# Optimization experiments

Hardware: AMD Instinct MI355X
Metric: run time of the kernel (lower is better)

## Reference

```python
import jax, jax.numpy as jnp
import numpy as np


def setup_inputs() -> dict:
    key = jax.random.key(0)
    ks = jax.random.split(key, 5)
    B, C, H, W = 8, 64, 64, 64
    Ci = 32  # inter_channels = in_channels // 2
    s = 1.0 / np.sqrt(C)
    return {
        "x": jax.random.normal(ks[0], (B, C, H, W), jnp.float32),
        "Wg": jax.random.normal(ks[1], (Ci, C), jnp.float32) * s,
        "bg": jnp.zeros((Ci,), jnp.float32),
        "Wt": jax.random.normal(ks[2], (Ci, C), jnp.float32) * s,
        "bt": jnp.zeros((Ci,), jnp.float32),
        "Wp": jax.random.normal(ks[3], (Ci, C), jnp.float32) * s,
        "bp": jnp.zeros((Ci,), jnp.float32),
        "Ww": jax.random.normal(ks[4], (C, Ci), jnp.float32) * (1.0 / np.sqrt(Ci)),
        "bw": jnp.zeros((C,), jnp.float32),
    }


def _proj(x, Wc, bc):
    # 1x1 conv: (B,C,H,W) -> (B,O,H,W), then flatten spatial -> (B,O,N)
    b, c, h, w = x.shape
    y = jnp.einsum("oc,bchw->bohw", Wc, x) + bc[None, :, None, None]
    return y.reshape(b, Wc.shape[0], h * w)


def reference(x, Wg, bg, Wt, bt, Wp, bp, Ww, bw):
    b, c, h, w = x.shape
    g_x = _proj(x, Wg, bg).transpose(0, 2, 1)      # (B, N, Ci)
    theta_x = _proj(x, Wt, bt).transpose(0, 2, 1)  # (B, N, Ci)
    phi_x = _proj(x, Wp, bp)                        # (B, Ci, N)
    f = jnp.einsum("bnd,bdm->bnm", theta_x, phi_x)  # (B, N, N)
    f_div_C = jax.nn.softmax(f, axis=-1)
    y = jnp.einsum("bnm,bmd->bnd", f_div_C, g_x)    # (B, N, Ci)
    y = y.transpose(0, 2, 1).reshape(b, Wg.shape[0], h, w)
    W_y = jnp.einsum("od,bdhw->bohw", Ww, y) + bw[None, :, None, None]
    return W_y + x
```

## Files before the change

### kernel.cpp

```cpp
#include <hip/hip_runtime.h>
#include <hip/hip_bf16.h>
#include <cstdint>
#include <cstddef>

#define B_ 8
#define C_ 64
#define CI 32
#define N_ 4096
#define LOG2E 1.44269504088896340736f

typedef __attribute__((ext_vector_type(8))) short bf16x8;
typedef __attribute__((ext_vector_type(4))) float f32x4;

static __device__ __forceinline__ ushort f2bf(float x) {
  union { float f; uint32_t u; } v; v.f = x;
  uint32_t r = v.u + 0x7FFFu + ((v.u >> 16) & 1u);
  return (ushort)(r >> 16);
}

static __device__ __forceinline__ uint32_t cvt_pk_bf16(float lo, float hi) {
  uint32_t r;
  asm("v_cvt_pk_bf16_f32 %0, %1, %2" : "=v"(r) : "v"(lo), "v"(hi));
  return r;
}

__global__ __launch_bounds__(256) void proj_kernel(
    const float* __restrict__ x,
    const float* __restrict__ Wg, const float* __restrict__ bg,
    const float* __restrict__ Wt, const float* __restrict__ bt,
    const float* __restrict__ Wp, const float* __restrict__ bp,
    ushort* __restrict__ theta_t, ushort* __restrict__ phi_t,
    ushort* __restrict__ gmat)
{
  __shared__ float WLt[C_ * CI];
  __shared__ float bL[CI];

  const int z = blockIdx.z;
  const float* W; const float* bias;
  if (z == 0)      { W = Wt; bias = bt; }
  else if (z == 1) { W = Wp; bias = bp; }
  else             { W = Wg; bias = bg; }

  const int t = threadIdx.x;
  #pragma unroll
  for (int k = 0; k < 8; ++k) {
    const int i = t + k * 256;
    WLt[(i % C_) * CI + (i / C_)] = W[i];
  }
  if (t < CI) bL[t] = bias[t];
  __syncthreads();

  const int b = blockIdx.y;
  const int n = blockIdx.x * 64 + (t & 63);
  const int dq = t >> 6;
  const float* xb = x + ((size_t)b * C_) * N_ + n;

  float acc[8];
  #pragma unroll
  for (int i = 0; i < 8; ++i) acc[i] = bL[dq * 8 + i];

  #pragma unroll 8
  for (int c = 0; c < C_; ++c) {
    const float xv = xb[(size_t)c * N_];
    const float4 w0 = *(const float4*)&WLt[c * CI + dq * 8];
    const float4 w1 = *(const float4*)&WLt[c * CI + dq * 8 + 4];
    acc[0] = fmaf(w0.x, xv, acc[0]);
    acc[1] = fmaf(w0.y, xv, acc[1]);
    acc[2] = fmaf(w0.z, xv, acc[2]);
    acc[3] = fmaf(w0.w, xv, acc[3]);
    acc[4] = fmaf(w1.x, xv, acc[4]);
    acc[5] = fmaf(w1.y, xv, acc[5]);
    acc[6] = fmaf(w1.z, xv, acc[6]);
    acc[7] = fmaf(w1.w, xv, acc[7]);
  }

  if (z == 2) {
    #pragma unroll
    for (int i = 0; i < 8; ++i)
      gmat[((size_t)(b * CI) + dq * 8 + i) * N_ + n] = f2bf(acc[i]);
  } else {
    const float scale = (z == 0) ? LOG2E : 1.0f;
    uint32_t w[4];
    #pragma unroll
    for (int k = 0; k < 4; ++k)
      w[k] = (uint32_t)f2bf(acc[2 * k] * scale) |
             ((uint32_t)f2bf(acc[2 * k + 1] * scale) << 16);
    ushort* base = (z == 0) ? theta_t : phi_t;
    *(uint4*)(base + ((size_t)(b * N_) + n) * CI + dq * 8) =
        make_uint4(w[0], w[1], w[2], w[3]);
  }
}

__global__ __launch_bounds__(512, 2) void attn_kernel(
    const ushort* __restrict__ theta_t,
    const ushort* __restrict__ phi_t,
    const ushort* __restrict__ gmat,
    const float* __restrict__ Ww, const float* __restrict__ bw,
    const float* __restrict__ x, float* __restrict__ out)
{
  __shared__ union {
    ushort pt[8][2][16 * 64];
    float  accS[4][32][64];
  } Sh;
  __shared__ float mlS[4][8][64];
  __shared__ float WwL[C_ * CI];
  __shared__ float Yl[32 * 66];

  const int tid = threadIdx.x;
  const int lane = tid & 63;
  const int mh = tid >> 6;
  const int bid = blockIdx.x;
  const int b = bid & 7;
  const int n0 = (bid >> 3) * 64;
  const int g4 = lane >> 4;
  const int c16 = lane & 15;
  const int sw = (c16 & 7) << 4;

  #pragma unroll
  for (int i = 0; i < 4; ++i) WwL[tid + i * 512] = Ww[tid + i * 512];

  bf16x8 qfrag[4];
  #pragma unroll
  for (int s = 0; s < 4; ++s)
    qfrag[s] = *(const bf16x8*)(theta_t +
        ((size_t)(b * N_ + n0 + s * 16 + c16)) * CI + g4 * 8);

  f32x4 acc[4][2];
  f32x4 cinit[4];
  #pragma unroll
  for (int s = 0; s < 4; ++s) {
    acc[s][0] = (f32x4){0.f, 0.f, 0.f, 0.f};
    acc[s][1] = (f32x4){0.f, 0.f, 0.f, 0.f};
    cinit[s]  = (f32x4){0.f, 0.f, 0.f, 0.f};
  }
  float l_lane[4] = {0.f, 0.f, 0.f, 0.f};

  const int mq0 = mh * 512;
  const ushort* kbase = phi_t + ((size_t)(b * N_ + mq0 + c16)) * CI + g4 * 8;
  const ushort* vb0 = gmat + ((size_t)(b * CI + c16)) * N_ + mq0 + g4 * 8;
  const ushort* vb1 = vb0 + (size_t)16 * N_;

  char* pw[2][4]; const char* prd[2][2];
  #pragma unroll
  for (int pb = 0; pb < 2; ++pb) {
    #pragma unroll
    for (int mt = 0; mt < 4; ++mt)
      pw[pb][mt] = (char*)Sh.pt[mh][pb] + ((c16 * 128 + mt * 32 + g4 * 8) ^ sw);
    #pragma unroll
    for (int ks = 0; ks < 2; ++ks)
      prd[pb][ks] = (const char*)Sh.pt[mh][pb] +
                    ((c16 * 128 + ks * 64 + g4 * 16) ^ sw);
  }

  bf16x8 kf[4], kfn[4], vf0[2], vf1[2];
  #pragma unroll
  for (int mt = 0; mt < 4; ++mt)
    kfn[mt] = *(const bf16x8*)(kbase + (size_t)(mt * 16) * CI);

  const int NT = 8;
  for (int t = 0; t < NT; ++t) {
    #pragma unroll
    for (int mt = 0; mt < 4; ++mt) kf[mt] = kfn[mt];
    const int tn = (t + 1 < NT) ? t + 1 : t;
    #pragma unroll
    for (int mt = 0; mt < 4; ++mt)
      kfn[mt] = *(const bf16x8*)(kbase + (size_t)(tn * 64 + mt * 16) * CI);
    #pragma unroll
    for (int ks = 0; ks < 2; ++ks) {
      vf0[ks] = *(const bf16x8*)(vb0 + t * 64 + ks * 32);
      vf1[ks] = *(const bf16x8*)(vb1 + t * 64 + ks * 32);
    }

    #pragma unroll
    for (int s = 0; s < 4; ++s) {
      const int pb = s & 1;
      f32x4 f[4];
      __builtin_amdgcn_s_setprio(1);
      #pragma unroll
      for (int mt = 0; mt < 4; ++mt)
        f[mt] = __builtin_amdgcn_mfma_f32_16x16x32_bf16(
            kf[mt], qfrag[s], cinit[s], 0, 0, 0);
      __builtin_amdgcn_s_setprio(0);

      float pv[4][4];
      #pragma unroll
      for (int mt = 0; mt < 4; ++mt) {
        #pragma unroll
        for (int rr = 0; rr < 4; ++rr)
          pv[mt][rr] = __builtin_amdgcn_exp2f(f[mt][rr]);
        l_lane[s] += (pv[mt][0] + pv[mt][1]) + (pv[mt][2] + pv[mt][3]);
      }
      #pragma unroll
      for (int mt = 0; mt < 4; ++mt) {
        uint2 wv;
        wv.x = cvt_pk_bf16(pv[mt][0], pv[mt][1]);
        wv.y = cvt_pk_bf16(pv[mt][2], pv[mt][3]);
        *(uint2*)pw[pb][mt] = wv;
      }
      asm volatile("s_waitcnt lgkmcnt(0)" ::: "memory");
      __builtin_amdgcn_sched_barrier(0);

      __builtin_amdgcn_s_setprio(1);
      #pragma unroll
      for (int ks = 0; ks < 2; ++ks) {
        const bf16x8 pfrag = *(const bf16x8*)prd[pb][ks];
        acc[s][0] = __builtin_amdgcn_mfma_f32_16x16x32_bf16(
            vf0[ks], pfrag, acc[s][0], 0, 0, 0);
        acc[s][1] = __builtin_amdgcn_mfma_f32_16x16x32_bf16(
            vf1[ks], pfrag, acc[s][1], 0, 0, 0);
      }
      __builtin_amdgcn_s_setprio(0);

      if (__any(l_lane[s] > 0x1p40f)) {
        const float sc = 0x1p-64f;
        acc[s][0] *= sc; acc[s][1] *= sc; l_lane[s] *= sc;
        #pragma unroll
        for (int rr = 0; rr < 4; ++rr) cinit[s][rr] -= 64.f;
      }
    }
  }

  float m_run[4];
  #pragma unroll
  for (int s = 0; s < 4; ++s) {
    l_lane[s] += __shfl_xor(l_lane[s], 16);
    l_lane[s] += __shfl_xor(l_lane[s], 32);
    m_run[s] = -cinit[s][0];
  }

  #pragma unroll
  for (int r = 4; r >= 1; r >>= 1) {
    __syncthreads();
    if (mh >= r && mh < 2 * r) {
      float* ad = &Sh.accS[mh - r][0][0] + lane;
      float* md = &mlS[mh - r][0][0] + lane;
      #pragma unroll
      for (int s = 0; s < 4; ++s) {
        #pragma unroll
        for (int rr = 0; rr < 4; ++rr) {
          ad[(s * 8 + rr) * 64]     = acc[s][0][rr];
          ad[(s * 8 + 4 + rr) * 64] = acc[s][1][rr];
        }
        md[s * 64]       = m_run[s];
        md[(4 + s) * 64] = l_lane[s];
      }
    }
    __syncthreads();
    if (mh < r) {
      const float* as_ = &Sh.accS[mh][0][0] + lane;
      const float* ms_ = &mlS[mh][0][0] + lane;
      #pragma unroll
      for (int s = 0; s < 4; ++s) {
        const float mb = ms_[s * 64];
        const float lb = ms_[(4 + s) * 64];
        const float mM = fmaxf(m_run[s], mb);
        const float ea = __builtin_amdgcn_exp2f(m_run[s] - mM);
        const float eb = __builtin_amdgcn_exp2f(mb - mM);
        #pragma unroll
        for (int rr = 0; rr < 4; ++rr) {
          acc[s][0][rr] = acc[s][0][rr] * ea + as_[(s * 8 + rr) * 64] * eb;
          acc[s][1][rr] = acc[s][1][rr] * ea + as_[(s * 8 + 4 + rr) * 64] * eb;
        }
        l_lane[s] = l_lane[s] * ea + lb * eb;
        m_run[s] = mM;
      }
    }
  }
  __syncthreads();

  if (mh == 0) {
    #pragma unroll
    for (int s = 0; s < 4; ++s) {
      const float inv = 1.0f / l_lane[s];
      const int q = s * 16 + c16;
      #pragma unroll
      for (int rr = 0; rr < 4; ++rr) {
        Yl[(g4 * 4 + rr) * 66 + q]      = acc[s][0][rr] * inv;
        Yl[(16 + g4 * 4 + rr) * 66 + q] = acc[s][1][rr] * inv;
      }
    }
  }
  __syncthreads();

  const int nl = tid & 63;
  const int cg = tid >> 6;
  float oacc[8];
  #pragma unroll
  for (int i = 0; i < 8; ++i) oacc[i] = bw[cg * 8 + i];
  #pragma unroll
  for (int d = 0; d < CI; ++d) {
    const float yv = Yl[d * 66 + nl];
    #pragma unroll
    for (int i = 0; i < 8; ++i)
      oacc[i] = fmaf(WwL[(cg * 8 + i) * CI + d], yv, oacc[i]);
  }
  #pragma unroll
  for (int i = 0; i < 8; ++i) {
    const size_t idx = ((size_t)(b * C_ + cg * 8 + i)) * N_ + n0 + nl;
    out[idx] = oacc[i] + x[idx];
  }
}

extern "C" void kernel_launch(void* const* d_in, const int* in_sizes, int n_in,
                              void* d_out, int out_size, void* d_ws, size_t ws_size,
                              hipStream_t stream) {
  const float* x  = (const float*)d_in[0];
  const float* Wg = (const float*)d_in[1];
  const float* bg = (const float*)d_in[2];
  const float* Wt = (const float*)d_in[3];
  const float* bt = (const float*)d_in[4];
  const float* Wp = (const float*)d_in[5];
  const float* bp = (const float*)d_in[6];
  const float* Ww = (const float*)d_in[7];
  const float* bw = (const float*)d_in[8];
  float* out = (float*)d_out;

  char* ws = (char*)d_ws;
  ushort* theta_t = (ushort*)(ws);
  ushort* phi_t   = (ushort*)(ws + (size_t)2 * 1024 * 1024);
  ushort* gmat    = (ushort*)(ws + (size_t)4 * 1024 * 1024);

  proj_kernel<<<dim3(N_ / 64, B_, 3), 256, 0, stream>>>(
      x, Wg, bg, Wt, bt, Wp, bp, theta_t, phi_t, gmat);
  attn_kernel<<<dim3((N_ / 64) * B_), 512, 0, stream>>>(
      theta_t, phi_t, gmat, Ww, bw, x, out);
}
```

Measured before the change: 60.36 us.

## Fuse three projections into one pass, prefetch V fragments, drop setprio

The projection kernel now computes theta, phi and g in one 512-thread block per spatial tile, so x is read once instead of three times. The grid loses its z dimension and each thread produces four outputs for each of the three projections. In the attention loop, V fragments are now prefetched one tile ahead, the same way K already was, to hide global load latency. The s_setprio hints around the MFMA sections are removed, which changes wave scheduling priority, and the extra prefetch registers may raise register pressure.

```diff
diff --git a/kernel.cpp b/kernel.cpp
--- a/kernel.cpp
+++ b/kernel.cpp
@@ -24,7 +24,7 @@
   return r;
 }
 
-__global__ __launch_bounds__(256) void proj_kernel(
+__global__ __launch_bounds__(512) void proj_kernel(
     const float* __restrict__ x,
     const float* __restrict__ Wg, const float* __restrict__ bg,
     const float* __restrict__ Wt, const float* __restrict__ bt,
@@ -32,63 +32,54 @@
     ushort* __restrict__ theta_t, ushort* __restrict__ phi_t,
     ushort* __restrict__ gmat)
 {
-  __shared__ float WLt[C_ * CI];
-  __shared__ float bL[CI];
-
-  const int z = blockIdx.z;
-  const float* W; const float* bias;
-  if (z == 0)      { W = Wt; bias = bt; }
-  else if (z == 1) { W = Wp; bias = bp; }
-  else             { W = Wg; bias = bg; }
+  __shared__ float WT[C_ * CI], WP[C_ * CI], WG[C_ * CI];
+  __shared__ float bT[CI], bP[CI], bG[CI];
 
   const int t = threadIdx.x;
   #pragma unroll
-  for (int k = 0; k < 8; ++k) {
-    const int i = t + k * 256;
-    WLt[(i % C_) * CI + (i / C_)] = W[i];
-  }
-  if (t < CI) bL[t] = bias[t];
+  for (int k = 0; k < 4; ++k) {
+    const int i = t + k * 512;
+    const int j = (i & 63) * CI + (i >> 6);
+    WT[j] = Wt[i]; WP[j] = Wp[i]; WG[j] = Wg[i];
+  }
+  if (t < CI) { bT[t] = bt[t]; bP[t] = bp[t]; bG[t] = bg[t]; }
   __syncthreads();
 
   const int b = blockIdx.y;
   const int n = blockIdx.x * 64 + (t & 63);
-  const int dq = t >> 6;
+  const int dg = t >> 6;
   const float* xb = x + ((size_t)b * C_) * N_ + n;
 
-  float acc[8];
-  #pragma unroll
-  for (int i = 0; i < 8; ++i) acc[i] = bL[dq * 8 + i];
+  float at[4], ap[4], ag[4];
+  #pragma unroll
+  for (int i = 0; i < 4; ++i) {
+    at[i] = bT[dg * 4 + i]; ap[i] = bP[dg * 4 + i]; ag[i] = bG[dg * 4 + i];
+  }
 
   #pragma unroll 8
   for (int c = 0; c < C_; ++c) {
     const float xv = xb[(size_t)c * N_];
-    const float4 w0 = *(const float4*)&WLt[c * CI + dq * 8];
-    const float4 w1 = *(const float4*)&WLt[c * CI + dq * 8 + 4];
-    acc[0] = fmaf(w0.x, xv, acc[0]);
-    acc[1] = fmaf(w0.y, xv, acc[1]);
-    acc[2] = fmaf(w0.z, xv, acc[2]);
-    acc[3] = fmaf(w0.w, xv, acc[3]);
-    acc[4] = fmaf(w1.x, xv, acc[4]);
-    acc[5] = fmaf(w1.y, xv, acc[5]);
-    acc[6] = fmaf(w1.z, xv, acc[6]);
-    acc[7] = fmaf(w1.w, xv, acc[7]);
-  }
-
-  if (z == 2) {
-    #pragma unroll
-    for (int i = 0; i < 8; ++i)
-      gmat[((size_t)(b * CI) + dq * 8 + i) * N_ + n] = f2bf(acc[i]);
-  } else {
-    const float scale = (z == 0) ? LOG2E : 1.0f;
-    uint32_t w[4];
-    #pragma unroll
-    for (int k = 0; k < 4; ++k)
-      w[k] = (uint32_t)f2bf(acc[2 * k] * scale) |
-             ((uint32_t)f2bf(acc[2 * k + 1] * scale) << 16);
-    ushort* base = (z == 0) ? theta_t : phi_t;
-    *(uint4*)(base + ((size_t)(b * N_) + n) * CI + dq * 8) =
-        make_uint4(w[0], w[1], w[2], w[3]);
-  }
+    const float4 wt4 = *(const float4*)&WT[c * CI + dg * 4];
+    const float4 wp4 = *(const float4*)&WP[c * CI + dg * 4];
+    const float4 wg4 = *(const float4*)&WG[c * CI + dg * 4];
+    at[0] = fmaf(wt4.x, xv, at[0]); at[1] = fmaf(wt4.y, xv, at[1]);
+    at[2] = fmaf(wt4.z, xv, at[2]); at[3] = fmaf(wt4.w, xv, at[3]);
+    ap[0] = fmaf(wp4.x, xv, ap[0]); ap[1] = fmaf(wp4.y, xv, ap[1]);
+    ap[2] = fmaf(wp4.z, xv, ap[2]); ap[3] = fmaf(wp4.w, xv, ap[3]);
+    ag[0] = fmaf(wg4.x, xv, ag[0]); ag[1] = fmaf(wg4.y, xv, ag[1]);
+    ag[2] = fmaf(wg4.z, xv, ag[2]); ag[3] = fmaf(wg4.w, xv, ag[3]);
+  }
+
+  uint2 wt2, wp2;
+  wt2.x = (uint32_t)f2bf(at[0] * LOG2E) | ((uint32_t)f2bf(at[1] * LOG2E) << 16);
+  wt2.y = (uint32_t)f2bf(at[2] * LOG2E) | ((uint32_t)f2bf(at[3] * LOG2E) << 16);
+  wp2.x = (uint32_t)f2bf(ap[0]) | ((uint32_t)f2bf(ap[1]) << 16);
+  wp2.y = (uint32_t)f2bf(ap[2]) | ((uint32_t)f2bf(ap[3]) << 16);
+  *(uint2*)(theta_t + ((size_t)(b * N_) + n) * CI + dg * 4) = wt2;
+  *(uint2*)(phi_t   + ((size_t)(b * N_) + n) * CI + dg * 4) = wp2;
+  #pragma unroll
+  for (int i = 0; i < 4; ++i)
+    gmat[((size_t)(b * CI) + dg * 4 + i) * N_ + n] = f2bf(ag[i]);
 }
 
 __global__ __launch_bounds__(512, 2) void attn_kernel(
@@ -152,35 +143,42 @@
                     ((c16 * 128 + ks * 64 + g4 * 16) ^ sw);
   }
 
-  bf16x8 kf[4], kfn[4], vf0[2], vf1[2];
+  bf16x8 kf[4], kfn[4], vf0[2], vf1[2], vfn0[2], vfn1[2];
   #pragma unroll
   for (int mt = 0; mt < 4; ++mt)
     kfn[mt] = *(const bf16x8*)(kbase + (size_t)(mt * 16) * CI);
+  #pragma unroll
+  for (int ks = 0; ks < 2; ++ks) {
+    vfn0[ks] = *(const bf16x8*)(vb0 + ks * 32);
+    vfn1[ks] = *(const bf16x8*)(vb1 + ks * 32);
+  }
 
   const int NT = 8;
   for (int t = 0; t < NT; ++t) {
     #pragma unroll
     for (int mt = 0; mt < 4; ++mt) kf[mt] = kfn[mt];
+    #pragma unroll
+    for (int ks = 0; ks < 2; ++ks) {
+      vf0[ks] = vfn0[ks]; vf1[ks] = vfn1[ks];
+    }
     const int tn = (t + 1 < NT) ? t + 1 : t;
     #pragma unroll
     for (int mt = 0; mt < 4; ++mt)
       kfn[mt] = *(const bf16x8*)(kbase + (size_t)(tn * 64 + mt * 16) * CI);
     #pragma unroll
     for (int ks = 0; ks < 2; ++ks) {
-      vf0[ks] = *(const bf16x8*)(vb0 + t * 64 + ks * 32);
-      vf1[ks] = *(const bf16x8*)(vb1 + t * 64 + ks * 32);
+      vfn0[ks] = *(const bf16x8*)(vb0 + tn * 64 + ks * 32);
+      vfn1[ks] = *(const bf16x8*)(vb1 + tn * 64 + ks * 32);
     }
 
     #pragma unroll
     for (int s = 0; s < 4; ++s) {
       const int pb = s & 1;
       f32x4 f[4];
-      __builtin_amdgcn_s_setprio(1);
       #pragma unroll
       for (int mt = 0; mt < 4; ++mt)
         f[mt] = __builtin_amdgcn_mfma_f32_16x16x32_bf16(
             kf[mt], qfrag[s], cinit[s], 0, 0, 0);
-      __builtin_amdgcn_s_setprio(0);
 
       float pv[4][4];
       #pragma unroll
@@ -200,7 +198,6 @@
       asm volatile("s_waitcnt lgkmcnt(0)" ::: "memory");
       __builtin_amdgcn_sched_barrier(0);
 
-      __builtin_amdgcn_s_setprio(1);
       #pragma unroll
       for (int ks = 0; ks < 2; ++ks) {
         const bf16x8 pfrag = *(const bf16x8*)prd[pb][ks];
@@ -209,7 +206,6 @@
         acc[s][1] = __builtin_amdgcn_mfma_f32_16x16x32_bf16(
             vf1[ks], pfrag, acc[s][1], 0, 0, 0);
       }
-      __builtin_amdgcn_s_setprio(0);
 
       if (__any(l_lane[s] > 0x1p40f)) {
         const float sc = 0x1p-64f;
@@ -320,7 +316,7 @@
   ushort* phi_t   = (ushort*)(ws + (size_t)2 * 1024 * 1024);
   ushort* gmat    = (ushort*)(ws + (size_t)4 * 1024 * 1024);
 
-  proj_kernel<<<dim3(N_ / 64, B_, 3), 256, 0, stream>>>(
+  proj_kernel<<<dim3(N_ / 64, B_), 512, 0, stream>>>(
       x, Wg, bg, Wt, bt, Wp, bp, theta_t, phi_t, gmat);
   attn_kernel<<<dim3((N_ / 64) * B_), 512, 0, stream>>>(
       theta_t, phi_t, gmat, Ww, bw, x, out);
```

New measurement: 61.51 us. About the same (+1.9%).
